# Kernel optimization log

Hardware: AMD Instinct MI355X
Metric: run time of the kernel (lower is better)

Reference implementation:

```python
import jax, jax.numpy as jnp
import numpy as np

VOCAB, EMB, HID, CAT = 50000, 256, 512, 5
K, N, R = 40, 5, 20
L, B = 400, 256


def setup_inputs() -> dict:
    key = jax.random.key(0)
    ks = jax.random.split(key, 16)
    s = 0.05
    u = jax.random.uniform(ks[11], (N, B, K + 1), minval=1e-6, maxval=1.0 - 1e-6)
    return {
        "xs": jax.random.randint(ks[0], (L, B), 0, VOCAB),
        "lengths": jnp.full((B,), L, dtype=jnp.int32),
        "t": jax.random.randint(ks[1], (B,), 0, CAT),
        "embed_W": jax.random.normal(ks[2], (VOCAB, EMB)) * s,
        "W_ih": jax.random.normal(ks[3], (4 * HID, EMB)) * s,
        "W_hh": jax.random.normal(ks[4], (4 * HID, HID)) * s,
        "b_ih": jnp.zeros((4 * HID,)),
        "b_hh": jnp.zeros((4 * HID,)),
        "W_out": jax.random.normal(ks[5], (CAT, HID)) * s,
        "b_out": jnp.zeros((CAT,)),
        "W_jump": jax.random.normal(ks[6], (K + 1, HID)) * s,
        "b_jump": jnp.zeros((K + 1,)),
        "W_base": jax.random.normal(ks[7], (1, HID)) * s,
        "b_base": jnp.zeros((1,)),
        # inverted-dropout mask, p=0.1 (fixed for determinism)
        "dropout_mask": (jax.random.bernoulli(ks[8], 0.9, (L, B, EMB)) / 0.9).astype(jnp.float32),
        # gumbel noise for categorical jump sampling (gumbel-max trick)
        "gumbel": -jnp.log(-jnp.log(u)),
    }


def reference(xs, lengths, t, embed_W, W_ih, W_hh, b_ih, b_hh, W_out, b_out,
              W_jump, b_jump, W_base, b_base, dropout_mask, gumbel):
    del lengths  # LSTMJump.forward takes but never uses lengths
    Lm, Bs = xs.shape
    hid = W_hh.shape[1]
    embs = embed_W[xs] * dropout_mask            # [L,B,E]
    cols = jnp.arange(Bs)
    bias = b_ih + b_hh

    def lstm_cell(x, h, c):                      # torch nn.LSTM gate order i,f,g,o
        gates = x @ W_ih.T + h @ W_hh.T + bias   # [B,4H]
        i, f, g, o = jnp.split(gates, 4, axis=-1)
        c2 = jax.nn.sigmoid(f) * c + jax.nn.sigmoid(i) * jnp.tanh(g)
        return jax.nn.sigmoid(o) * jnp.tanh(c2), c2

    def maybe_step(h, c, rows):                  # masked single-step LSTM (_maybe_lstm)
        fp = rows >= Lm                          # feed_previous
        rows_eff = jnp.where(fp, Lm - 1, rows)
        h2, c2 = lstm_cell(embs[rows_eff, cols], h, c)
        m = fp[:, None]
        return jnp.where(m, h, h2), jnp.where(m, c, c2), fp, rows_eff

    def inner(carry, _):
        h, c, rows = carry
        h, c, _, rows_eff = maybe_step(h, c, rows)
        return (h, c, rows_eff + 1), None

    def outer(carry, g_n):
        h, c, rows = carry
        (h, c, rows), _ = jax.lax.scan(inner, (h, c, rows), None, length=R)
        h, c, fp, rows_eff = maybe_step(h, c, rows)
        logp = jax.nn.log_softmax(h @ W_jump.T + b_jump, axis=1)   # [B,K+1]
        jump = jnp.argmax(logp + g_n, axis=1).astype(rows.dtype)   # Categorical sample
        lp = jnp.take_along_axis(logp, jump[:, None], axis=1)[:, 0]
        lp = jnp.where(fp, 0.0, lp)
        base = (h @ W_base.T + b_base)[:, 0]
        rows = jnp.where(jump == 0, Lm, rows_eff + jump)
        return (h, c, rows), (lp, base)

    h0 = jnp.zeros((Bs, hid), dtype=embs.dtype)
    rows0 = jnp.zeros((Bs,), dtype=jnp.int32)
    (h, c, _), (log_probs, baselines) = jax.lax.scan(outer, (h0, h0, rows0), gumbel)
    # log_probs, baselines: [N,B]

    y = jax.nn.log_softmax(h @ W_out.T + b_out, axis=1)            # [B,CAT]
    nll = -jnp.mean(jnp.take_along_axis(y, t[:, None], axis=1))
    reward = jax.lax.stop_gradient(jnp.where(jnp.argmax(y, axis=1) == t, 1.0, -1.0))  # [B]
    reinforce = jnp.mean(-(reward[None, :] - baselines) * log_probs)
    mse = jnp.sum((baselines - reward[None, :]) ** 2)              # size_average=False
    return nll + reinforce + mse
```

## Files before the change

kernel.cpp:

```cpp
#include <hip/hip_runtime.h>

#define LSEQ 400
#define BATCH 256
#define EMBD 256
#define HIDD 512
#define KDIM 768
#define NJ 41
#define RLX __ATOMIC_RELAXED
#define AGT __HIP_MEMORY_SCOPE_AGENT

typedef __attribute__((ext_vector_type(8))) short short8x;
typedef __attribute__((ext_vector_type(4))) float f32x4;
typedef __attribute__((ext_vector_type(4))) unsigned int u32x4;
typedef unsigned long long u64;

union BQ { short8x v; unsigned short u[8]; u64 q[2]; };
union BX { u32x4 v; unsigned short u[8]; u64 q[2]; };

__device__ __forceinline__ float bf2f(unsigned short u) {
    union { unsigned int i; float f; } v; v.i = ((unsigned int)u) << 16; return v.f;
}
__device__ __forceinline__ unsigned short f2bf(float f) {
    union { float f; unsigned int i; } v; v.f = f;
    unsigned int x = v.i;
    return (unsigned short)((x + 0x7fffu + ((x >> 16) & 1u)) >> 16);
}
__device__ __forceinline__ float sigm(float x) { return 1.0f / (1.0f + __expf(-x)); }

__device__ __forceinline__ void ast(u64* p, u64 v) {
    __hip_atomic_store(p, v, RLX, AGT);
}
#define ALD16(dst, addr) \
    asm volatile("global_load_dwordx4 %0, %1, off sc1" : "=&v"(dst) : "v"(addr) : "memory")

__global__ __launch_bounds__(256) void prologue_kernel(
    const float* __restrict__ W_ih, const float* __restrict__ W_hh,
    const int* __restrict__ xs, const float* __restrict__ embW,
    const float* __restrict__ mask,
    unsigned short* __restrict__ pW, unsigned short* __restrict__ xh0,
    int* __restrict__ base_rows, unsigned* __restrict__ flags)
{
    int wid = blockIdx.x, t = threadIdx.x;
    int lane = t & 63, subw = t >> 6;
    int gw = wid * 4 + subw;
    for (int q = 0; q < 3; ++q) {
        int f = gw * 3 + q;
        int rg = f / 192, r1 = f % 192;
        int w = r1 / 48,  r2 = r1 % 48;
        int m = r2 / 24,  kt = r2 % 24;
        int grow = w * 512 + rg * 32 + m * 16 + (lane & 15);
        int k0 = kt * 32 + ((lane >> 4) << 3);
        BQ pk;
        #pragma unroll
        for (int j = 0; j < 8; ++j) {
            int k = k0 + j;
            float wv = (k < EMBD) ? W_ih[(size_t)grow * EMBD + k]
                                  : W_hh[(size_t)grow * HIDD + (k - EMBD)];
            pk.u[j] = f2bf(wv);
        }
        ((short8x*)pW)[((size_t)f) * 64 + lane] = pk.v;
    }
    int b = wid;
    int tok = xs[b];
    float ev = embW[(size_t)tok * EMBD + t] * mask[(size_t)b * EMBD + t];
    xh0[(size_t)b * KDIM + t] = f2bf(ev);
    for (int e = t; e < HIDD; e += 256) xh0[(size_t)b * KDIM + EMBD + e] = 0;
    if (t == 0) base_rows[b] = 0;
    if (t < 32) flags[wid * 32 + t] = 0u;
}

__global__ __launch_bounds__(256, 1) void persistent_kernel(
    const unsigned short* __restrict__ pW,
    unsigned short* __restrict__ xh,
    int* __restrict__ base_rows,
    const float* __restrict__ b_ih, const float* __restrict__ b_hh,
    const int* __restrict__ xs, const float* __restrict__ embW,
    const float* __restrict__ mask,
    const float* __restrict__ W_jump, const float* __restrict__ b_jump,
    const float* __restrict__ W_base, const float* __restrict__ b_base,
    const float* __restrict__ gumbel,
    float* __restrict__ lp_arr, float* __restrict__ base_arr,
    const float* __restrict__ W_out, const float* __restrict__ b_out,
    const int* __restrict__ tcls,
    float* __restrict__ loss_arr, unsigned* __restrict__ flags)
{
    __shared__ u64 Bsh[16 * 193];
    __shared__ float gates[4][32][17];
    __shared__ __align__(8) unsigned short hstage[16][32];
    __shared__ __align__(8) unsigned short xstage[256];
    __shared__ float zsh[42];
    __shared__ int rowsh, nbrsh;

    const int wg = blockIdx.x;
    const int cb = wg >> 4, rg = wg & 15;
    const int C0 = cb * 16;
    const int colg = C0 + rg;
    const int tid = threadIdx.x, lane = tid & 63, w = tid >> 6;

    short8x A[48];
    {
        const short8x* Ab = ((const short8x*)pW) + ((size_t)(rg * 4 + w) * 48) * 64 + lane;
        #pragma unroll
        for (int f = 0; f < 48; ++f) A[f] = Ab[f * 64];
    }

    const int u = tid >> 3;
    const int c0 = (tid & 7) << 1;
    const int hid = rg * 32 + u;
    const float bi  = b_ih[hid]        + b_hh[hid];
    const float bf_ = b_ih[512 + hid]  + b_hh[512 + hid];
    const float bgt = b_ih[1024 + hid] + b_hh[1024 + hid];
    const float bo  = b_ih[1536 + hid] + b_hh[1536 + hid];

    float cf0 = 0.f, cf1 = 0.f, hf0 = 0.f, hf1 = 0.f;
    int brc0 = 0, brc1 = 0, rowg = 0;

    unsigned bar = 0;
    const size_t XH = (size_t)BATCH * KDIM;
    int p = 0;

    for (int n = 0; n < 5; ++n) {
        for (int i = 0; i <= 20; ++i) {
            const unsigned short* xin  = xh + (size_t)p * XH;
            unsigned short*       xout = xh + (size_t)(p ^ 1) * XH;

            float ge = 0.f, gm = 0.f;
            if (i < 20) {
                int row = rowg + i + 1; if (row > LSEQ - 1) row = LSEQ - 1;
                int tok = xs[(size_t)row * BATCH + colg];
                ge = embW[(size_t)tok * EMBD + tid];
                gm = mask[((size_t)row * BATCH + colg) * EMBD + tid];
            }

            {
                const unsigned char* gb = (const unsigned char*)(xin + (size_t)C0 * KDIM);
                BX tmp[6];
                #pragma unroll
                for (int j = 0; j < 6; ++j)
                    ALD16(tmp[j].v, gb + ((size_t)(j * 256 + tid) << 4));
                asm volatile("s_waitcnt vmcnt(0)" ::: "memory");
                __builtin_amdgcn_sched_barrier(0);
                #pragma unroll
                for (int j = 0; j < 6; ++j) {
                    unsigned g = (unsigned)(j * 256 + tid);
                    unsigned col = g / 96u, o16 = g % 96u;
                    u64* d = &Bsh[col * 193u + o16 * 2u];
                    d[0] = tmp[j].q[0];
                    d[1] = tmp[j].q[1];
                }
            }
            __syncthreads();

            f32x4 e0 = {0,0,0,0}, o0 = {0,0,0,0};
            f32x4 e1 = {0,0,0,0}, o1 = {0,0,0,0};
            {
                const u64* bc = &Bsh[(size_t)(lane & 15) * 193 + ((lane >> 4) << 1)];
                #pragma unroll
                for (int kt = 0; kt < 24; kt += 2) {
                    BQ qe, qo;
                    qe.q[0] = bc[kt * 8];     qe.q[1] = bc[kt * 8 + 1];
                    qo.q[0] = bc[kt * 8 + 8]; qo.q[1] = bc[kt * 8 + 9];
                    e0 = __builtin_amdgcn_mfma_f32_16x16x32_bf16(A[kt],          qe.v, e0, 0, 0, 0);
                    e1 = __builtin_amdgcn_mfma_f32_16x16x32_bf16(A[24 + kt],     qe.v, e1, 0, 0, 0);
                    o0 = __builtin_amdgcn_mfma_f32_16x16x32_bf16(A[kt + 1],      qo.v, o0, 0, 0, 0);
                    o1 = __builtin_amdgcn_mfma_f32_16x16x32_bf16(A[24 + kt + 1], qo.v, o1, 0, 0, 0);
                }
            }
            f32x4 acc0 = e0 + o0, acc1 = e1 + o1;
            {
                int ur = (lane >> 4) << 2;
                int cl = lane & 15;
                #pragma unroll
                for (int v = 0; v < 4; ++v) {
                    gates[w][ur + v][cl]      = acc0[v];
                    gates[w][16 + ur + v][cl] = acc1[v];
                }
            }
            __syncthreads();

            {
                bool fp = (brc0 + i) >= LSEQ;
                float gi = gates[0][u][c0] + bi;
                float gf = gates[1][u][c0] + bf_;
                float gc = gates[2][u][c0] + bgt;
                float go = gates[3][u][c0] + bo;
                float c2 = sigm(gf) * cf0 + sigm(gi) * tanhf(gc);
                float h2 = sigm(go) * tanhf(c2);
                if (!fp) { cf0 = c2; hf0 = h2; }
                hstage[c0][u] = f2bf(hf0);
            }
            {
                bool fp = (brc1 + i) >= LSEQ;
                float gi = gates[0][u][c0 + 1] + bi;
                float gf = gates[1][u][c0 + 1] + bf_;
                float gc = gates[2][u][c0 + 1] + bgt;
                float go = gates[3][u][c0 + 1] + bo;
                float c2 = sigm(gf) * cf1 + sigm(gi) * tanhf(gc);
                float h2 = sigm(go) * tanhf(c2);
                if (!fp) { cf1 = c2; hf1 = h2; }
                hstage[c0 + 1][u] = f2bf(hf1);
            }
            if (i < 20) xstage[tid] = f2bf(ge * gm);
            __syncthreads();

            if (tid < 128) {
                int col = tid >> 3, qd = tid & 7;
                u64 hv = ((const u64*)&hstage[col][0])[qd];
                ast((u64*)(xout + (size_t)(C0 + col) * KDIM + EMBD + rg * 32) + qd, hv);
            }
            if (i < 20 && tid < 64) {
                ast((u64*)(xout + (size_t)colg * KDIM) + tid, ((const u64*)xstage)[tid]);
            }
            p ^= 1;

            ++bar;
            asm volatile("s_waitcnt vmcnt(0) lgkmcnt(0)" ::: "memory");
            __syncthreads();
            if (tid == 0) __hip_atomic_store(&flags[wg * 32], bar, RLX, AGT);
            if (tid < 16) {
                while (__hip_atomic_load(&flags[(cb * 16 + tid) * 32], RLX, AGT) < bar)
                    __builtin_amdgcn_s_sleep(1);
            }
            __syncthreads();

            if (i == 20) {
                unsigned short* xcur = xh + (size_t)p * XH;
                BX hv;
                {
                    const unsigned char* hq =
                        (const unsigned char*)(xcur + (size_t)colg * KDIM + EMBD + lane * 8);
                    ALD16(hv.v, hq);
                    asm volatile("s_waitcnt vmcnt(0)" ::: "memory");
                    __builtin_amdgcn_sched_barrier(0);
                }
                float hf[8];
                #pragma unroll
                for (int q = 0; q < 8; ++q) hf[q] = bf2f(hv.u[q]);

                for (int r = w; r < 42; r += 4) {
                    const float* wr = (r < NJ) ? (W_jump + (size_t)r * HIDD) : W_base;
                    const float4* wp = (const float4*)(wr + lane * 8);
                    float4 w0 = wp[0], w1 = wp[1];
                    float acc = w0.x*hf[0] + w0.y*hf[1] + w0.z*hf[2] + w0.w*hf[3]
                              + w1.x*hf[4] + w1.y*hf[5] + w1.z*hf[6] + w1.w*hf[7];
                    #pragma unroll
                    for (int off = 32; off > 0; off >>= 1) acc += __shfl_down(acc, off, 64);
                    if (lane == 0) zsh[r] = acc + ((r < NJ) ? b_jump[r] : b_base[0]);
                }
                __syncthreads();

                if (tid == 0) {
                    const float* g = gumbel + ((size_t)n * BATCH + colg) * NJ;
                    float m = -1e30f, mg = -1e30f; int jm = 0;
                    for (int r = 0; r < NJ; ++r) {
                        float z = zsh[r];
                        if (z > m) m = z;
                        float zg = z + g[r];
                        if (zg > mg) { mg = zg; jm = r; }
                    }
                    float s = 0.0f;
                    for (int r = 0; r < NJ; ++r) s += expf(zsh[r] - m);
                    float lse = m + logf(s);
                    int br = rowg;
                    bool fp = (br + 20) >= LSEQ;
                    lp_arr[n * BATCH + colg]   = fp ? 0.0f : (zsh[jm] - lse);
                    base_arr[n * BATCH + colg] = zsh[41];
                    int reff = br + 20; if (reff > LSEQ - 1) reff = LSEQ - 1;
                    int nbr = (jm == 0) ? LSEQ : (reff + jm);
                    __hip_atomic_store(&base_rows[colg], nbr, RLX, AGT);
                    nbrsh = nbr;
                    rowsh = (nbr > LSEQ - 1) ? (LSEQ - 1) : nbr;
                }
                __syncthreads();

                if (n < 4) {
                    int row = rowsh;
                    int tok = xs[(size_t)row * BATCH + colg];
                    float ev = embW[(size_t)tok * EMBD + tid] *
                               mask[((size_t)row * BATCH + colg) * EMBD + tid];
                    xstage[tid] = f2bf(ev);
                }
                rowg = nbrsh;
                __syncthreads();
                if (n < 4 && tid < 64) {
                    ast((u64*)(xcur + (size_t)colg * KDIM) + tid, ((const u64*)xstage)[tid]);
                }

                ++bar;
                asm volatile("s_waitcnt vmcnt(0) lgkmcnt(0)" ::: "memory");
                __syncthreads();
                if (tid == 0) __hip_atomic_store(&flags[wg * 32], bar, RLX, AGT);
                if (tid < 16) {
                    while (__hip_atomic_load(&flags[(cb * 16 + tid) * 32], RLX, AGT) < bar)
                        __builtin_amdgcn_s_sleep(1);
                }
                __syncthreads();
                brc0 = __hip_atomic_load(&base_rows[C0 + c0],     RLX, AGT);
                brc1 = __hip_atomic_load(&base_rows[C0 + c0 + 1], RLX, AGT);
            }
        }
    }

    {
        const unsigned short* xcur = xh + (size_t)p * XH;
        BX hv;
        {
            const unsigned char* hq =
                (const unsigned char*)(xcur + (size_t)colg * KDIM + EMBD + lane * 8);
            ALD16(hv.v, hq);
            asm volatile("s_waitcnt vmcnt(0)" ::: "memory");
            __builtin_amdgcn_sched_barrier(0);
        }
        float hf[8];
        #pragma unroll
        for (int q = 0; q < 8; ++q) hf[q] = bf2f(hv.u[q]);

        for (int r = w; r < 5; r += 4) {
            const float4* wp = (const float4*)(W_out + (size_t)r * HIDD + lane * 8);
            float4 w0 = wp[0], w1 = wp[1];
            float acc = w0.x*hf[0] + w0.y*hf[1] + w0.z*hf[2] + w0.w*hf[3]
                      + w1.x*hf[4] + w1.y*hf[5] + w1.z*hf[6] + w1.w*hf[7];
            #pragma unroll
            for (int off = 32; off > 0; off >>= 1) acc += __shfl_down(acc, off, 64);
            if (lane == 0) zsh[r] = acc + b_out[r];
        }
        __syncthreads();

        if (tid == 0) {
            float y[5];
            #pragma unroll
            for (int c = 0; c < 5; ++c) y[c] = zsh[c];
            float m = y[0]; int am = 0;
            for (int c = 1; c < 5; ++c) if (y[c] > m) { m = y[c]; am = c; }
            float s = 0.0f;
            for (int c = 0; c < 5; ++c) s += expf(y[c] - m);
            float lse = m + logf(s);
            int tb = tcls[colg];
            float nll_p  = -(y[tb] - lse) * (1.0f / BATCH);
            float reward = (am == tb) ? 1.0f : -1.0f;
            float rp = 0.0f, mp = 0.0f;
            for (int nn = 0; nn < 5; ++nn) {
                float bs = base_arr[nn * BATCH + colg];
                float lp = lp_arr[nn * BATCH + colg];
                rp += -(reward - bs) * lp;
                float d = bs - reward;
                mp += d * d;
            }
            loss_arr[colg] = nll_p + rp * (1.0f / (5.0f * BATCH)) + mp;
        }
    }
}

__global__ __launch_bounds__(256) void reduce_kernel(
    const float* __restrict__ loss_arr, float* __restrict__ out)
{
    __shared__ float red[256];
    int t = threadIdx.x;
    red[t] = loss_arr[t];
    __syncthreads();
    for (int off = 128; off > 0; off >>= 1) {
        if (t < off) red[t] += red[t + off];
        __syncthreads();
    }
    if (t == 0) out[0] = red[0];
}

extern "C" void kernel_launch(void* const* d_in, const int* in_sizes, int n_in,
                              void* d_out, int out_size, void* d_ws, size_t ws_size,
                              hipStream_t stream)
{
    (void)in_sizes; (void)n_in; (void)out_size; (void)ws_size;
    const int*   xs     = (const int*)d_in[0];
    const int*   tcls   = (const int*)d_in[2];
    const float* embW   = (const float*)d_in[3];
    const float* W_ih   = (const float*)d_in[4];
    const float* W_hh   = (const float*)d_in[5];
    const float* b_ih   = (const float*)d_in[6];
    const float* b_hh   = (const float*)d_in[7];
    const float* W_out  = (const float*)d_in[8];
    const float* b_out  = (const float*)d_in[9];
    const float* W_jump = (const float*)d_in[10];
    const float* b_jump = (const float*)d_in[11];
    const float* W_base = (const float*)d_in[12];
    const float* b_base = (const float*)d_in[13];
    const float* mask   = (const float*)d_in[14];
    const float* gumbel = (const float*)d_in[15];

    char* wsp = (char*)d_ws;
    unsigned short* pW  = (unsigned short*)(wsp);
    unsigned short* xh  = (unsigned short*)(wsp + 3145728);
    int*      base_rows = (int*)(wsp + 3932160);
    float*    lp_arr    = (float*)(wsp + 3933184);
    float*    base_arr  = (float*)(wsp + 3938304);
    float*    loss_arr  = (float*)(wsp + 3943424);
    unsigned* flags     = (unsigned*)(wsp + 3944448);
    float*    outp      = (float*)d_out;

    prologue_kernel<<<256, 256, 0, stream>>>(W_ih, W_hh, xs, embW, mask,
                                             pW, xh, base_rows, flags);

    void* args[] = {
        (void*)&pW, (void*)&xh, (void*)&base_rows,
        (void*)&b_ih, (void*)&b_hh, (void*)&xs, (void*)&embW, (void*)&mask,
        (void*)&W_jump, (void*)&b_jump, (void*)&W_base, (void*)&b_base,
        (void*)&gumbel, (void*)&lp_arr, (void*)&base_arr,
        (void*)&W_out, (void*)&b_out, (void*)&tcls,
        (void*)&loss_arr, (void*)&flags
    };
    hipError_t err = hipLaunchCooperativeKernel((const void*)persistent_kernel,
                                                dim3(256), dim3(256), args, 0, stream);
    if (err != hipSuccess) {
        persistent_kernel<<<256, 256, 0, stream>>>(
            pW, xh, base_rows, b_ih, b_hh, xs, embW, mask,
            W_jump, b_jump, W_base, b_base, gumbel, lp_arr, base_arr,
            W_out, b_out, tcls, loss_arr, flags);
    }
    reduce_kernel<<<1, 256, 0, stream>>>(loss_arr, outp);
}
```

Measured before the change: 497.3 us.

## Gather embeddings locally and overlap input-projection MFMAs with cross-block barrier wait

Each workgroup now gathers and packs the embedding×mask slice for its own 16 columns directly into shared memory instead of exchanging it through the global xh buffer. The global exchange buffer shrinks to hidden state only. The x-part of the gate matmul (first 8 k-tiles) is issued before spinning on the inter-block flags, so the wait now overlaps with compute. This cuts global traffic and shortens the critical path per step, at the cost of redundant embedding gathers across the 16 row-group blocks and more complex barrier placement.

```diff
diff --git a/kernel.cpp b/kernel.cpp
--- a/kernel.cpp
+++ b/kernel.cpp
@@ -4,7 +4,6 @@
 #define BATCH 256
 #define EMBD 256
 #define HIDD 512
-#define KDIM 768
 #define NJ 41
 #define RLX __ATOMIC_RELAXED
 #define AGT __HIP_MEMORY_SCOPE_AGENT
@@ -26,18 +25,19 @@
     return (unsigned short)((x + 0x7fffu + ((x >> 16) & 1u)) >> 16);
 }
 __device__ __forceinline__ float sigm(float x) { return 1.0f / (1.0f + __expf(-x)); }
-
-__device__ __forceinline__ void ast(u64* p, u64 v) {
-    __hip_atomic_store(p, v, RLX, AGT);
-}
+__device__ __forceinline__ u64 pack4(float4 e, float4 m) {
+    return (u64)f2bf(e.x * m.x) | ((u64)f2bf(e.y * m.y) << 16)
+         | ((u64)f2bf(e.z * m.z) << 32) | ((u64)f2bf(e.w * m.w) << 48);
+}
+
 #define ALD16(dst, addr) \
     asm volatile("global_load_dwordx4 %0, %1, off sc1" : "=&v"(dst) : "v"(addr) : "memory")
+#define AST16(addr, src) \
+    asm volatile("global_store_dwordx4 %0, %1, off sc1" :: "v"(addr), "v"(src) : "memory")
 
 __global__ __launch_bounds__(256) void prologue_kernel(
     const float* __restrict__ W_ih, const float* __restrict__ W_hh,
-    const int* __restrict__ xs, const float* __restrict__ embW,
-    const float* __restrict__ mask,
-    unsigned short* __restrict__ pW, unsigned short* __restrict__ xh0,
+    unsigned short* __restrict__ pW, unsigned short* __restrict__ hbuf,
     int* __restrict__ base_rows, unsigned* __restrict__ flags)
 {
     int wid = blockIdx.x, t = threadIdx.x;
@@ -60,18 +60,14 @@
         }
         ((short8x*)pW)[((size_t)f) * 64 + lane] = pk.v;
     }
-    int b = wid;
-    int tok = xs[b];
-    float ev = embW[(size_t)tok * EMBD + t] * mask[(size_t)b * EMBD + t];
-    xh0[(size_t)b * KDIM + t] = f2bf(ev);
-    for (int e = t; e < HIDD; e += 256) xh0[(size_t)b * KDIM + EMBD + e] = 0;
-    if (t == 0) base_rows[b] = 0;
+    if (t < 128) ((u64*)hbuf)[(size_t)wid * 128 + t] = 0ull;
+    if (t == 0) base_rows[wid] = 0;
     if (t < 32) flags[wid * 32 + t] = 0u;
 }
 
 __global__ __launch_bounds__(256, 1) void persistent_kernel(
     const unsigned short* __restrict__ pW,
-    unsigned short* __restrict__ xh,
+    unsigned short* __restrict__ hbuf,
     int* __restrict__ base_rows,
     const float* __restrict__ b_ih, const float* __restrict__ b_hh,
     const int* __restrict__ xs, const float* __restrict__ embW,
@@ -87,9 +83,8 @@
     __shared__ u64 Bsh[16 * 193];
     __shared__ float gates[4][32][17];
     __shared__ __align__(8) unsigned short hstage[16][32];
-    __shared__ __align__(8) unsigned short xstage[256];
+    __shared__ int brs[16];
     __shared__ float zsh[42];
-    __shared__ int rowsh, nbrsh;
 
     const int wg = blockIdx.x;
     const int cb = wg >> 4, rg = wg & 15;
@@ -112,59 +107,90 @@
     const float bgt = b_ih[1024 + hid] + b_hh[1024 + hid];
     const float bo  = b_ih[1536 + hid] + b_hh[1536 + hid];
 
+    const int gcol = tid >> 4, gseg = tid & 15;
+    u64* const gdst = &Bsh[(size_t)gcol * 193 + gseg * 4];
+
+    const u64* const bc = &Bsh[(size_t)(lane & 15) * 193 + ((lane >> 4) << 1)];
+
     float cf0 = 0.f, cf1 = 0.f, hf0 = 0.f, hf1 = 0.f;
-    int brc0 = 0, brc1 = 0, rowg = 0;
+    int brc0 = 0, brc1 = 0;
 
     unsigned bar = 0;
-    const size_t XH = (size_t)BATCH * KDIM;
+    const size_t HB = (size_t)BATCH * HIDD;
     int p = 0;
+
+    if (tid < 16) brs[tid] = 0;
+    __syncthreads();
+    {
+        int tok = xs[C0 + gcol];
+        const float4* ep = (const float4*)(embW + (size_t)tok * EMBD + gseg * 16);
+        const float4* mp = (const float4*)(mask + ((size_t)(C0 + gcol)) * EMBD + gseg * 16);
+        #pragma unroll
+        for (int s = 0; s < 4; ++s) gdst[s] = pack4(ep[s], mp[s]);
+    }
+    __syncthreads();
 
     for (int n = 0; n < 5; ++n) {
         for (int i = 0; i <= 20; ++i) {
-            const unsigned short* xin  = xh + (size_t)p * XH;
-            unsigned short*       xout = xh + (size_t)(p ^ 1) * XH;
-
-            float ge = 0.f, gm = 0.f;
-            if (i < 20) {
-                int row = rowg + i + 1; if (row > LSEQ - 1) row = LSEQ - 1;
-                int tok = xs[(size_t)row * BATCH + colg];
-                ge = embW[(size_t)tok * EMBD + tid];
-                gm = mask[((size_t)row * BATCH + colg) * EMBD + tid];
-            }
+            const unsigned short* hin  = hbuf + (size_t)p * HB;
+            unsigned short*       hout = hbuf + (size_t)(p ^ 1) * HB;
+
+            f32x4 e0 = {0,0,0,0}, o0 = {0,0,0,0};
+            f32x4 e1 = {0,0,0,0}, o1 = {0,0,0,0};
+            #pragma unroll
+            for (int kt = 0; kt < 8; kt += 2) {
+                BQ qe, qo;
+                qe.q[0] = bc[kt * 8];     qe.q[1] = bc[kt * 8 + 1];
+                qo.q[0] = bc[kt * 8 + 8]; qo.q[1] = bc[kt * 8 + 9];
+                e0 = __builtin_amdgcn_mfma_f32_16x16x32_bf16(A[kt],          qe.v, e0, 0, 0, 0);
+                e1 = __builtin_amdgcn_mfma_f32_16x16x32_bf16(A[24 + kt],     qe.v, e1, 0, 0, 0);
+                o0 = __builtin_amdgcn_mfma_f32_16x16x32_bf16(A[kt + 1],      qo.v, o0, 0, 0, 0);
+                o1 = __builtin_amdgcn_mfma_f32_16x16x32_bf16(A[24 + kt + 1], qo.v, o1, 0, 0, 0);
+            }
+
+            if (tid < 16) {
+                while (__hip_atomic_load(&flags[(cb * 16 + tid) * 32], RLX, AGT) < bar)
+                    __builtin_amdgcn_s_sleep(1);
+            }
+            __syncthreads();
 
             {
-                const unsigned char* gb = (const unsigned char*)(xin + (size_t)C0 * KDIM);
-                BX tmp[6];
-                #pragma unroll
-                for (int j = 0; j < 6; ++j)
-                    ALD16(tmp[j].v, gb + ((size_t)(j * 256 + tid) << 4));
+                const unsigned char* hb = (const unsigned char*)(hin + (size_t)C0 * HIDD);
+                BX tmp[4];
+                #pragma unroll
+                for (int j = 0; j < 4; ++j)
+                    ALD16(tmp[j].v, hb + ((size_t)(j * 256 + tid) << 4));
                 asm volatile("s_waitcnt vmcnt(0)" ::: "memory");
                 __builtin_amdgcn_sched_barrier(0);
                 #pragma unroll
-                for (int j = 0; j < 6; ++j) {
+                for (int j = 0; j < 4; ++j) {
                     unsigned g = (unsigned)(j * 256 + tid);
-                    unsigned col = g / 96u, o16 = g % 96u;
-                    u64* d = &Bsh[col * 193u + o16 * 2u];
+                    u64* d = &Bsh[(g >> 6) * 193u + 64u + (g & 63u) * 2u];
                     d[0] = tmp[j].q[0];
                     d[1] = tmp[j].q[1];
                 }
             }
             __syncthreads();
 
-            f32x4 e0 = {0,0,0,0}, o0 = {0,0,0,0};
-            f32x4 e1 = {0,0,0,0}, o1 = {0,0,0,0};
-            {
-                const u64* bc = &Bsh[(size_t)(lane & 15) * 193 + ((lane >> 4) << 1)];
-                #pragma unroll
-                for (int kt = 0; kt < 24; kt += 2) {
-                    BQ qe, qo;
-                    qe.q[0] = bc[kt * 8];     qe.q[1] = bc[kt * 8 + 1];
-                    qo.q[0] = bc[kt * 8 + 8]; qo.q[1] = bc[kt * 8 + 9];
-                    e0 = __builtin_amdgcn_mfma_f32_16x16x32_bf16(A[kt],          qe.v, e0, 0, 0, 0);
-                    e1 = __builtin_amdgcn_mfma_f32_16x16x32_bf16(A[24 + kt],     qe.v, e1, 0, 0, 0);
-                    o0 = __builtin_amdgcn_mfma_f32_16x16x32_bf16(A[kt + 1],      qo.v, o0, 0, 0, 0);
-                    o1 = __builtin_amdgcn_mfma_f32_16x16x32_bf16(A[24 + kt + 1], qo.v, o1, 0, 0, 0);
-                }
+            float4 ge[4], gm[4];
+            if (i < 20) {
+                int row = brs[gcol] + i + 1; if (row > LSEQ - 1) row = LSEQ - 1;
+                int tok = xs[(size_t)row * BATCH + C0 + gcol];
+                const float4* ep = (const float4*)(embW + (size_t)tok * EMBD + gseg * 16);
+                const float4* mp = (const float4*)(mask + ((size_t)row * BATCH + C0 + gcol) * EMBD + gseg * 16);
+                #pragma unroll
+                for (int s = 0; s < 4; ++s) { ge[s] = ep[s]; gm[s] = mp[s]; }
+            }
+
+            #pragma unroll
+            for (int kt = 8; kt < 24; kt += 2) {
+                BQ qe, qo;
+                qe.q[0] = bc[kt * 8];     qe.q[1] = bc[kt * 8 + 1];
+                qo.q[0] = bc[kt * 8 + 8]; qo.q[1] = bc[kt * 8 + 9];
+                e0 = __builtin_amdgcn_mfma_f32_16x16x32_bf16(A[kt],          qe.v, e0, 0, 0, 0);
+                e1 = __builtin_amdgcn_mfma_f32_16x16x32_bf16(A[24 + kt],     qe.v, e1, 0, 0, 0);
+                o0 = __builtin_amdgcn_mfma_f32_16x16x32_bf16(A[kt + 1],      qo.v, o0, 0, 0, 0);
+                o1 = __builtin_amdgcn_mfma_f32_16x16x32_bf16(A[24 + kt + 1], qo.v, o1, 0, 0, 0);
             }
             f32x4 acc0 = e0 + o0, acc1 = e1 + o1;
             {
@@ -200,39 +226,36 @@
                 if (!fp) { cf1 = c2; hf1 = h2; }
                 hstage[c0 + 1][u] = f2bf(hf1);
             }
-            if (i < 20) xstage[tid] = f2bf(ge * gm);
+            if (i < 20) {
+                #pragma unroll
+                for (int s = 0; s < 4; ++s) gdst[s] = pack4(ge[s], gm[s]);
+            }
             __syncthreads();
 
-            if (tid < 128) {
-                int col = tid >> 3, qd = tid & 7;
-                u64 hv = ((const u64*)&hstage[col][0])[qd];
-                ast((u64*)(xout + (size_t)(C0 + col) * KDIM + EMBD + rg * 32) + qd, hv);
-            }
-            if (i < 20 && tid < 64) {
-                ast((u64*)(xout + (size_t)colg * KDIM) + tid, ((const u64*)xstage)[tid]);
+            if (tid < 64) {
+                int col = tid >> 2, part = tid & 3;
+                const u64* hs = (const u64*)&hstage[col][0];
+                BX v; v.q[0] = hs[part * 2]; v.q[1] = hs[part * 2 + 1];
+                unsigned short* dst = hout + (size_t)(C0 + col) * HIDD + rg * 32 + part * 16;
+                AST16(dst, v.v);
             }
             p ^= 1;
-
             ++bar;
             asm volatile("s_waitcnt vmcnt(0) lgkmcnt(0)" ::: "memory");
             __syncthreads();
             if (tid == 0) __hip_atomic_store(&flags[wg * 32], bar, RLX, AGT);
-            if (tid < 16) {
-                while (__hip_atomic_load(&flags[(cb * 16 + tid) * 32], RLX, AGT) < bar)
-                    __builtin_amdgcn_s_sleep(1);
-            }
-            __syncthreads();
 
             if (i == 20) {
-                unsigned short* xcur = xh + (size_t)p * XH;
+                if (tid < 16) {
+                    while (__hip_atomic_load(&flags[(cb * 16 + tid) * 32], RLX, AGT) < bar)
+                        __builtin_amdgcn_s_sleep(1);
+                }
+                __syncthreads();
+                const unsigned short* hcur = hbuf + (size_t)p * HB;
                 BX hv;
-                {
-                    const unsigned char* hq =
-                        (const unsigned char*)(xcur + (size_t)colg * KDIM + EMBD + lane * 8);
-                    ALD16(hv.v, hq);
-                    asm volatile("s_waitcnt vmcnt(0)" ::: "memory");
-                    __builtin_amdgcn_sched_barrier(0);
-                }
+                ALD16(hv.v, (const unsigned char*)(hcur + (size_t)colg * HIDD + lane * 8));
+                asm volatile("s_waitcnt vmcnt(0)" ::: "memory");
+                __builtin_amdgcn_sched_barrier(0);
                 float hf[8];
                 #pragma unroll
                 for (int q = 0; q < 8; ++q) hf[q] = bf2f(hv.u[q]);
@@ -261,30 +284,15 @@
                     float s = 0.0f;
                     for (int r = 0; r < NJ; ++r) s += expf(zsh[r] - m);
                     float lse = m + logf(s);
-                    int br = rowg;
+                    int br = brs[rg];
                     bool fp = (br + 20) >= LSEQ;
                     lp_arr[n * BATCH + colg]   = fp ? 0.0f : (zsh[jm] - lse);
                     base_arr[n * BATCH + colg] = zsh[41];
                     int reff = br + 20; if (reff > LSEQ - 1) reff = LSEQ - 1;
                     int nbr = (jm == 0) ? LSEQ : (reff + jm);
                     __hip_atomic_store(&base_rows[colg], nbr, RLX, AGT);
-                    nbrsh = nbr;
-                    rowsh = (nbr > LSEQ - 1) ? (LSEQ - 1) : nbr;
-                }
-                __syncthreads();
-
-                if (n < 4) {
-                    int row = rowsh;
-                    int tok = xs[(size_t)row * BATCH + colg];
-                    float ev = embW[(size_t)tok * EMBD + tid] *
-                               mask[((size_t)row * BATCH + colg) * EMBD + tid];
-                    xstage[tid] = f2bf(ev);
-                }
-                rowg = nbrsh;
-                __syncthreads();
-                if (n < 4 && tid < 64) {
-                    ast((u64*)(xcur + (size_t)colg * KDIM) + tid, ((const u64*)xstage)[tid]);
-                }
+                }
+                __syncthreads();
 
                 ++bar;
                 asm volatile("s_waitcnt vmcnt(0) lgkmcnt(0)" ::: "memory");
@@ -295,22 +303,30 @@
                         __builtin_amdgcn_s_sleep(1);
                 }
                 __syncthreads();
-                brc0 = __hip_atomic_load(&base_rows[C0 + c0],     RLX, AGT);
-                brc1 = __hip_atomic_load(&base_rows[C0 + c0 + 1], RLX, AGT);
+                if (tid < 16)
+                    brs[tid] = __hip_atomic_load(&base_rows[C0 + tid], RLX, AGT);
+                __syncthreads();
+                brc0 = brs[c0];
+                brc1 = brs[c0 + 1];
+                if (n < 4) {
+                    int row = brs[gcol]; if (row > LSEQ - 1) row = LSEQ - 1;
+                    int tok = xs[(size_t)row * BATCH + C0 + gcol];
+                    const float4* ep = (const float4*)(embW + (size_t)tok * EMBD + gseg * 16);
+                    const float4* mp = (const float4*)(mask + ((size_t)row * BATCH + C0 + gcol) * EMBD + gseg * 16);
+                    #pragma unroll
+                    for (int s = 0; s < 4; ++s) gdst[s] = pack4(ep[s], mp[s]);
+                }
+                __syncthreads();
             }
         }
     }
 
     {
-        const unsigned short* xcur = xh + (size_t)p * XH;
+        const unsigned short* hcur = hbuf + (size_t)p * HB;
         BX hv;
-        {
-            const unsigned char* hq =
-                (const unsigned char*)(xcur + (size_t)colg * KDIM + EMBD + lane * 8);
-            ALD16(hv.v, hq);
-            asm volatile("s_waitcnt vmcnt(0)" ::: "memory");
-            __builtin_amdgcn_sched_barrier(0);
-        }
+        ALD16(hv.v, (const unsigned char*)(hcur + (size_t)colg * HIDD + lane * 8));
+        asm volatile("s_waitcnt vmcnt(0)" ::: "memory");
+        __builtin_amdgcn_sched_barrier(0);
         float hf[8];
         #pragma unroll
         for (int q = 0; q < 8; ++q) hf[q] = bf2f(hv.u[q]);
@@ -388,19 +404,18 @@
 
     char* wsp = (char*)d_ws;
     unsigned short* pW  = (unsigned short*)(wsp);
-    unsigned short* xh  = (unsigned short*)(wsp + 3145728);
-    int*      base_rows = (int*)(wsp + 3932160);
-    float*    lp_arr    = (float*)(wsp + 3933184);
-    float*    base_arr  = (float*)(wsp + 3938304);
-    float*    loss_arr  = (float*)(wsp + 3943424);
-    unsigned* flags     = (unsigned*)(wsp + 3944448);
+    unsigned short* hbuf= (unsigned short*)(wsp + 3145728);
+    int*      base_rows = (int*)(wsp + 3670016);
+    float*    lp_arr    = (float*)(wsp + 3671040);
+    float*    base_arr  = (float*)(wsp + 3676160);
+    float*    loss_arr  = (float*)(wsp + 3681280);
+    unsigned* flags     = (unsigned*)(wsp + 3682304);
     float*    outp      = (float*)d_out;
 
-    prologue_kernel<<<256, 256, 0, stream>>>(W_ih, W_hh, xs, embW, mask,
-                                             pW, xh, base_rows, flags);
+    prologue_kernel<<<256, 256, 0, stream>>>(W_ih, W_hh, pW, hbuf, base_rows, flags);
 
     void* args[] = {
-        (void*)&pW, (void*)&xh, (void*)&base_rows,
+        (void*)&pW, (void*)&hbuf, (void*)&base_rows,
         (void*)&b_ih, (void*)&b_hh, (void*)&xs, (void*)&embW, (void*)&mask,
         (void*)&W_jump, (void*)&b_jump, (void*)&W_base, (void*)&b_base,
         (void*)&gumbel, (void*)&lp_arr, (void*)&base_arr,
@@ -411,7 +426,7 @@
                                                 dim3(256), dim3(256), args, 0, stream);
     if (err != hipSuccess) {
         persistent_kernel<<<256, 256, 0, stream>>>(
-            pW, xh, base_rows, b_ih, b_hh, xs, embW, mask,
+            pW, hbuf, base_rows, b_ih, b_hh, xs, embW, mask,
             W_jump, b_jump, W_base, b_base, gumbel, lp_arr, base_arr,
             W_out, b_out, tcls, loss_arr, flags);
     }
```

New measurement: 483.6 us. 2.8% less time.
